# Kernel tuning notes

Measured on AMD Instinct MI355X. Metric: run time of the kernel, lower is better.

The kernel has to match this reference:

```python
import jax, jax.numpy as jnp
import numpy as np

DIM = 512
HEADS = 8
HEAD_DIM = 64
MAX_FREQ = 256.0


def axial_freqs(H, W, head_dim, max_freq=MAX_FREQ):
    # rotary-embedding-torch: per-axis rotary dim = head_dim // 2, freqs_for='pixel'
    r = head_dim // 2
    base = jnp.linspace(1.0, max_freq / 2.0, r // 2) * jnp.pi  # (r/2,)
    ph = jnp.linspace(-1.0, 1.0, H)
    pw = jnp.linspace(-1.0, 1.0, W)
    fh = jnp.repeat(ph[:, None] * base[None, :], 2, axis=-1)  # (H, r) interleaved repeat
    fw = jnp.repeat(pw[:, None] * base[None, :], 2, axis=-1)  # (W, r)
    fh = jnp.broadcast_to(fh[:, None, :], (H, W, r))
    fw = jnp.broadcast_to(fw[None, :, :], (H, W, r))
    return jnp.concatenate([fh, fw], axis=-1)  # (H, W, head_dim)


def rotate_half(t):
    # interleaved pairs: (x1, x2) -> (-x2, x1)
    shp = t.shape
    t = t.reshape(*shp[:-1], -1, 2)
    return jnp.stack((-t[..., 1], t[..., 0]), axis=-1).reshape(shp)


def apply_rope(t, freqs):
    # freqs: (H, W, d) broadcast over (BT, h, H, W, d)
    return t * jnp.cos(freqs) + rotate_half(t) * jnp.sin(freqs)


def setup_inputs() -> dict:
    key = jax.random.key(0)
    k1, k2, k3 = jax.random.split(key, 3)
    B, T, H, W, D = 2, 8, 32, 32, DIM
    inner = HEADS * HEAD_DIM
    x = jax.random.normal(k1, (B, T, H, W, D), dtype=jnp.float32)
    w_qkv = jax.random.normal(k2, (3 * inner, D), dtype=jnp.float32) * (D ** -0.5)
    w_out = jax.random.normal(k3, (D, inner), dtype=jnp.float32) * (inner ** -0.5)
    b_out = jnp.zeros((D,), dtype=jnp.float32)
    return {"x": x, "w_qkv": w_qkv, "w_out": w_out, "b_out": b_out}


def reference(x, w_qkv, w_out, b_out):
    B, T, H, W, D = x.shape
    h, d = HEADS, HEAD_DIM
    qkv = jnp.einsum('bthwc,fc->bthwf', x, w_qkv)  # (B,T,H,W,3*inner)
    q, k, v = jnp.split(qkv, 3, axis=-1)

    def to_heads(t):
        # B T H W (h d) -> (B T) h H W d
        t = t.reshape(B * T, H, W, h, d)
        return jnp.transpose(t, (0, 3, 1, 2, 4))

    q, k, v = to_heads(q), to_heads(k), to_heads(v)
    freqs = axial_freqs(H, W, d)
    q = apply_rope(q, freqs)
    k = apply_rope(k, freqs)

    q = q.reshape(B * T, h, H * W, d)
    k = k.reshape(B * T, h, H * W, d)
    v = v.reshape(B * T, h, H * W, d)

    scale = d ** -0.5
    logits = jnp.einsum('bhnd,bhmd->bhnm', q, k) * scale
    attn = jax.nn.softmax(logits, axis=-1)
    out = jnp.einsum('bhnm,bhmd->bhnd', attn, v)  # (BT, h, HW, d)

    # (B T) h (H W) d -> B T H W (h d)
    out = out.reshape(B, T, h, H, W, d)
    out = jnp.transpose(out, (0, 1, 3, 4, 2, 5)).reshape(B, T, H, W, h * d)
    return jnp.einsum('bthwf,df->bthwd', out, w_out) + b_out
```

## Files before the change

### kernel.cpp

```cpp
#include <hip/hip_runtime.h>
#include <math.h>

#define NH 8
#define HD 64
#define NSEQ 1024
#define DMODEL 512
#define F3 1536
#define NTOK 16384
#define BH 128
#define KVP 72
#define TP 136
#define QSCALE 0.1803368867f

typedef __attribute__((ext_vector_type(8))) short bf16x8;
typedef __attribute__((ext_vector_type(4))) float f32x4;
typedef __attribute__((ext_vector_type(16))) float f32x16;
typedef __attribute__((ext_vector_type(4))) unsigned int u32x4;
#define MFMA16(a, b, c) __builtin_amdgcn_mfma_f32_16x16x32_bf16(a, b, c, 0, 0, 0)
#define MFMA32(a, b, c) __builtin_amdgcn_mfma_f32_32x32x16_bf16(a, b, c, 0, 0, 0)

__device__ __forceinline__ float freq_of(int j) {
    return 3.14159265358979323846f * (1.0f + (float)j * (127.0f / 15.0f));
}
__device__ __forceinline__ unsigned short bf16_hi(float x) {
    unsigned u = __builtin_bit_cast(unsigned, x);
    return (unsigned short)(u >> 16);
}
__device__ __forceinline__ unsigned short bf16_rtn(float x) {
    unsigned u = __builtin_bit_cast(unsigned, x);
    return (unsigned short)((u + 0x7FFF + ((u >> 16) & 1)) >> 16);
}
__device__ __forceinline__ float bf16_tofloat(unsigned short h) {
    unsigned u = ((unsigned)h) << 16;
    return __builtin_bit_cast(float, u);
}
__device__ __forceinline__ int swz(int r) { return (r & 3) ^ ((r >> 2) & 3); }

__global__ __launch_bounds__(256) void split_kernel(
        const float* __restrict__ src, unsigned short* __restrict__ hi,
        unsigned short* __restrict__ lo) {
    const int i = blockIdx.x * 256 + threadIdx.x;
    const float4 v = ((const float4*)src)[i];
    ushort4 h, l;
    h.x = bf16_hi(v.x); l.x = bf16_hi(v.x - bf16_tofloat(h.x));
    h.y = bf16_hi(v.y); l.y = bf16_hi(v.y - bf16_tofloat(h.y));
    h.z = bf16_hi(v.z); l.z = bf16_hi(v.z - bf16_tofloat(h.z));
    h.w = bf16_hi(v.w); l.w = bf16_hi(v.w - bf16_tofloat(h.w));
    ((ushort4*)hi)[i] = h;
    ((ushort4*)lo)[i] = l;
}
__global__ __launch_bounds__(256) void cvt_kernel(
        const float* __restrict__ src, unsigned short* __restrict__ dst) {
    const int i = blockIdx.x * 256 + threadIdx.x;
    const float4 v = ((const float4*)src)[i];
    ((ushort4*)dst)[i] = make_ushort4(bf16_rtn(v.x), bf16_rtn(v.y),
                                      bf16_rtn(v.z), bf16_rtn(v.w));
}

template<int PLANES, int NREP>
__device__ __forceinline__ void gemm_reg_pipe(
        const unsigned short* __restrict__ a_hi, const unsigned short* __restrict__ a_lo,
        const unsigned short* __restrict__ b_bf,
        char* lds, int m0, int f0, int t, f32x4 (&acc)[NREP][4][4]) {
    const int w = t >> 6, lane = t & 63, l15 = lane & 15, quad = lane >> 4;
    const int mw = (w & 1) * 64, nw = (w >> 1) * 64;
    const int APL = PLANES - 1;
    const int NPL = APL + NREP;
    const int STAGE = NPL * 4096;
    const int r = t >> 1;
    const int g0 = (t & 1) * 2;

    uint4 regs[NPL][2];
    auto load_regs = [&](int kt) {
        const int k0 = kt * 32;
        #pragma unroll
        for (int p = 0; p < NPL; p++) {
            const unsigned short* src = (p < APL) ? (p == 0 ? a_hi : a_lo) : b_bf;
            const int row0 = (p < APL) ? m0 : (f0 + (p - APL) * 128);
            const unsigned short* g = src + (size_t)(row0 + r) * DMODEL + k0 + g0 * 8;
            regs[p][0] = *(const uint4*)g;
            regs[p][1] = *(const uint4*)(g + 8);
        }
    };
    auto store_lds = [&](int stage) {
        unsigned short* S = (unsigned short*)lds + stage * STAGE;
        const int s0 = ((g0 ^ swz(r))) * 8;
        const int s1 = (((g0 + 1) ^ swz(r))) * 8;
        #pragma unroll
        for (int p = 0; p < NPL; p++) {
            unsigned short* Sp = S + p * 4096 + r * 32;
            *(uint4*)&Sp[s0] = regs[p][0];
            *(uint4*)&Sp[s1] = regs[p][1];
        }
    };

    load_regs(0);
    store_lds(0);
    for (int kt = 0; kt < 16; kt++) {
        __syncthreads();
        if (kt < 15) load_regs(kt + 1);
        const unsigned short* S = (const unsigned short*)lds + (kt & 1) * STAGE;
        bf16x8 ah[4], al[4];
        #pragma unroll
        for (int mt = 0; mt < 4; mt++) {
            const int rr = mw + mt * 16 + l15;
            const int off = rr * 32 + (quad ^ swz(rr)) * 8;
            ah[mt] = *(const bf16x8*)&S[off];
            if (APL == 2) al[mt] = *(const bf16x8*)&S[4096 + off];
        }
        #pragma unroll
        for (int nr = 0; nr < NREP; nr++) {
            bf16x8 bb[4];
            #pragma unroll
            for (int nt = 0; nt < 4; nt++) {
                const int rr = nw + nt * 16 + l15;
                bb[nt] = *(const bf16x8*)&S[(APL + nr) * 4096 + rr * 32
                                            + (quad ^ swz(rr)) * 8];
            }
            #pragma unroll
            for (int mt = 0; mt < 4; mt++)
                #pragma unroll
                for (int nt = 0; nt < 4; nt++) {
                    acc[nr][mt][nt] = MFMA16(ah[mt], bb[nt], acc[nr][mt][nt]);
                    if (APL == 2) acc[nr][mt][nt] = MFMA16(al[mt], bb[nt], acc[nr][mt][nt]);
                }
        }
        if (kt < 15) store_lds((kt + 1) & 1);
    }
    __syncthreads();
}

__global__ __launch_bounds__(256, 2) void qkv_mfma_kernel(
        const unsigned short* __restrict__ x_hi, const unsigned short* __restrict__ x_lo,
        const unsigned short* __restrict__ wq_bf,
        unsigned short* __restrict__ q_bf, unsigned short* __restrict__ k_bf,
        unsigned short* __restrict__ v_th) {
    __shared__ __align__(16) char lds[65536 + 4608];
    unsigned short* T = (unsigned short*)lds;
    float* t_cy = (float*)(lds + 65536);
    float* t_sy = t_cy + 64;
    float* t_cx = t_sy + 64;
    float* t_sx = t_cx + 512;

    const int m0 = blockIdx.x * 128;
    const int f0 = blockIdx.y * 256;
    const int t = threadIdx.x;
    const int w = t >> 6, lane = t & 63, l15 = lane & 15, quad = lane >> 4;
    const int mw = (w & 1) * 64, nw = (w >> 1) * 64;
    const int sel = f0 >> 9;
    const int bt = m0 >> 10;
    const int n0 = m0 & 1023;

    if (sel != 2) {
        for (int idx = t; idx < 576; idx += 256) {
            if (idx < 64) {
                const int yi = idx >> 4, j = idx & 15;
                const float pos = -1.0f + (float)((n0 >> 5) + yi) * (2.0f / 31.0f);
                float sv, cv; sincosf(pos * freq_of(j), &sv, &cv);
                t_sy[idx] = sv; t_cy[idx] = cv;
            } else {
                const int k2 = idx - 64, xi = k2 >> 4, j = k2 & 15;
                const float pos = -1.0f + (float)xi * (2.0f / 31.0f);
                float sv, cv; sincosf(pos * freq_of(j), &sv, &cv);
                t_sx[k2] = sv; t_cx[k2] = cv;
            }
        }
    }
    __syncthreads();

    f32x4 acc[2][4][4];
    #pragma unroll
    for (int nr = 0; nr < 2; nr++)
        #pragma unroll
        for (int mt = 0; mt < 4; mt++)
            #pragma unroll
            for (int nt = 0; nt < 4; nt++) acc[nr][mt][nt] = (f32x4){0.f, 0.f, 0.f, 0.f};

    gemm_reg_pipe<3, 2>(x_hi, x_lo, wq_bf, lds, m0, f0, t, acc);

    #pragma unroll
    for (int nr = 0; nr < 2; nr++) {
        const int fs = f0 + nr * 128;
        if (sel != 2) {
            const float post = (sel == 0) ? QSCALE : 1.0f;
            #pragma unroll
            for (int mt = 0; mt < 4; mt++)
                #pragma unroll
                for (int nt = 0; nt < 4; nt++)
                    #pragma unroll
                    for (int rr = 0; rr < 4; rr++) {
                        const int ml = mw + mt * 16 + quad * 4 + rr;
                        const int dd = (nw + nt * 16 + l15) & 63;
                        const int j0 = (dd & 31) >> 1;
                        float c, s;
                        if (dd < 32) { c = t_cy[(ml >> 5) * 16 + j0]; s = t_sy[(ml >> 5) * 16 + j0]; }
                        else         { c = t_cx[(ml & 31) * 16 + j0]; s = t_sx[(ml & 31) * 16 + j0]; }
                        const float v = acc[nr][mt][nt][rr];
                        const float pv = __shfl_xor(v, 1);
                        acc[nr][mt][nt][rr] =
                            ((l15 & 1) ? (v * c + pv * s) : (v * c - pv * s)) * post;
                    }
        }

        if (sel == 2) {
            #pragma unroll
            for (int mt = 0; mt < 4; mt++)
                #pragma unroll
                for (int nt = 0; nt < 4; nt++) {
                    const int fl = nw + nt * 16 + l15;
                    const int mlb = mw + mt * 16 + quad * 4;
                    ushort4 pk = make_ushort4(
                        bf16_rtn(acc[nr][mt][nt][0]), bf16_rtn(acc[nr][mt][nt][1]),
                        bf16_rtn(acc[nr][mt][nt][2]), bf16_rtn(acc[nr][mt][nt][3]));
                    *(ushort4*)&T[fl * TP + mlb] = pk;
                }
        } else {
            #pragma unroll
            for (int mt = 0; mt < 4; mt++)
                #pragma unroll
                for (int nt = 0; nt < 4; nt++)
                    #pragma unroll
                    for (int rr = 0; rr < 4; rr++) {
                        const int ml = mw + mt * 16 + quad * 4 + rr;
                        const int fl = nw + nt * 16 + l15;
                        T[ml * TP + fl] = bf16_rtn(acc[nr][mt][nt][rr]);
                    }
        }
        __syncthreads();
        if (sel == 2) {
            #pragma unroll
            for (int p = 0; p < 8; p++) {
                const int idx = p * 256 + t;
                const int fl = idx >> 4, g8 = (idx & 15) * 8;
                const int head = ((fs + fl) >> 6) & 7;
                *(uint4*)(v_th + ((size_t)(bt * NH + head) * HD + ((fs + fl) & 63)) * NSEQ
                          + n0 + g8) = *(const uint4*)&T[fl * TP + g8];
            }
        } else {
            unsigned short* dst = (sel == 0) ? q_bf : k_bf;
            #pragma unroll
            for (int p = 0; p < 8; p++) {
                const int idx = p * 256 + t;
                const int ml = idx >> 4, g8 = (idx & 15) * 8;
                const int head = ((fs + g8) >> 6) & 7;
                *(uint4*)(dst + ((size_t)(bt * NH + head) * NSEQ + n0 + ml) * HD
                          + ((fs + g8) & 63)) = *(const uint4*)&T[ml * TP + g8];
            }
        }
        __syncthreads();
    }
}

__global__ __launch_bounds__(256, 3) void attn_kernel(
        const unsigned short* __restrict__ q_bf, const unsigned short* __restrict__ k_bf,
        const unsigned short* __restrict__ v_th,
        unsigned short* __restrict__ o_bf) {
    __shared__ unsigned short Ks[2][64 * KVP];
    __shared__ unsigned short Vs[2][64 * KVP];

    const int bh = blockIdx.x;
    const int qt = blockIdx.y;
    const int t = threadIdx.x;
    const int w = t >> 6;
    const int lane = t & 63;
    const int l31 = lane & 31;
    const int hi = lane >> 5;

    const size_t bh_nd = (size_t)bh * NSEQ * HD;
    const size_t bh_dn = (size_t)bh * HD * NSEQ;

    bf16x8 qfB[4];
    {
        const size_t rbase = bh_nd + (size_t)(qt * 128 + w * 32 + l31) * HD + hi * 8;
        #pragma unroll
        for (int ds = 0; ds < 4; ds++)
            qfB[ds] = *(const bf16x8*)(q_bf + rbase + ds * 16);
    }

    uint4 kr[2], vr[2];
    auto load_kv = [&](int kt) {
        #pragma unroll
        for (int p = 0; p < 2; p++) {
            const int cc = t + p * 256;
            const int r = cc >> 3, off8 = (cc & 7) * 8;
            kr[p] = *(const uint4*)(k_bf + bh_nd + (size_t)(kt * 64 + r) * HD + off8);
            vr[p] = *(const uint4*)(v_th + bh_dn + (size_t)r * NSEQ + kt * 64 + off8);
        }
    };
    auto store_kv = [&](int st) {
        #pragma unroll
        for (int p = 0; p < 2; p++) {
            const int cc = t + p * 256;
            const int r = cc >> 3, off8 = (cc & 7) * 8;
            *(uint4*)&Ks[st][r * KVP + off8] = kr[p];
            *(uint4*)&Vs[st][r * KVP + off8] = vr[p];
        }
    };

    const bf16x8 ones = {(short)0x3F80, (short)0x3F80, (short)0x3F80, (short)0x3F80,
                         (short)0x3F80, (short)0x3F80, (short)0x3F80, (short)0x3F80};

    f32x16 o_acc[2], l_acc;
    #pragma unroll
    for (int i = 0; i < 16; i++) {
        o_acc[0][i] = 0.f; o_acc[1][i] = 0.f; l_acc[i] = 0.f;
    }

    load_kv(0);
    store_kv(0);
    for (int kt = 0; kt < 16; kt++) {
        __syncthreads();
        if (kt < 15) load_kv(kt + 1);
        const unsigned short* K = Ks[kt & 1];
        const unsigned short* V = Vs[kt & 1];

        #pragma unroll
        for (int nt2 = 0; nt2 < 2; nt2++) {
            f32x16 s;
            #pragma unroll
            for (int i = 0; i < 16; i++) s[i] = 0.f;
            #pragma unroll
            for (int ds = 0; ds < 4; ds++) {
                const bf16x8 kb =
                    *(const bf16x8*)&K[(nt2 * 32 + l31) * KVP + ds * 16 + hi * 8];
                s = MFMA32(kb, qfB[ds], s);
            }

            unsigned wv[8];
            #pragma unroll
            for (int i = 0; i < 8; i++) {
                const float p0 = exp2f(s[2 * i]);
                const float p1 = exp2f(s[2 * i + 1]);
                asm("v_cvt_pk_bf16_f32 %0, %1, %2" : "=v"(wv[i]) : "v"(p0), "v"(p1));
            }
            asm volatile("v_permlane32_swap_b32 %0, %1" : "+v"(wv[0]), "+v"(wv[2]));
            asm volatile("v_permlane32_swap_b32 %0, %1" : "+v"(wv[1]), "+v"(wv[3]));
            asm volatile("v_permlane32_swap_b32 %0, %1" : "+v"(wv[4]), "+v"(wv[6]));
            asm volatile("v_permlane32_swap_b32 %0, %1" : "+v"(wv[5]), "+v"(wv[7]));

            #pragma unroll
            for (int k2 = 0; k2 < 2; k2++) {
                const u32x4 paw = {wv[k2 * 4 + 0], wv[k2 * 4 + 1],
                                   wv[k2 * 4 + 2], wv[k2 * 4 + 3]};
                const bf16x8 pa = __builtin_bit_cast(bf16x8, paw);
                const int kstep = nt2 * 2 + k2;
                l_acc = MFMA32(pa, ones, l_acc);
                #pragma unroll
                for (int dt = 0; dt < 2; dt++) {
                    const bf16x8 vb =
                        *(const bf16x8*)&V[(dt * 32 + l31) * KVP + kstep * 16 + hi * 8];
                    o_acc[dt] = MFMA32(pa, vb, o_acc[dt]);
                }
            }
        }
        if (kt < 15) store_kv((kt + 1) & 1);
    }

    __syncthreads();
    unsigned short* Osh = &Ks[0][0];
    #pragma unroll
    for (int r = 0; r < 16; r++) {
        const float inv = 1.0f / l_acc[r];
        const int row = w * 32 + (r & 3) + 8 * (r >> 2) + 4 * hi;
        #pragma unroll
        for (int dt = 0; dt < 2; dt++)
            Osh[row * KVP + dt * 32 + l31] = bf16_rtn(o_acc[dt][r] * inv);
    }
    __syncthreads();
    const int btq = bh >> 3, head = bh & 7;
    #pragma unroll
    for (int p = 0; p < 4; p++) {
        const int idx = p * 256 + t;
        const int row = idx >> 3, g8 = (idx & 7) * 8;
        *(uint4*)(o_bf + ((size_t)(btq * NSEQ + qt * 128 + row)) * DMODEL
                  + head * HD + g8) = *(const uint4*)&Osh[row * KVP + g8];
    }
}

__global__ __launch_bounds__(256, 3) void proj_mfma_kernel(
        const unsigned short* __restrict__ o_bf,
        const unsigned short* __restrict__ wo_bf,
        const float* __restrict__ b_out, float* __restrict__ out) {
    __shared__ __align__(16) char lds[32768];

    const int m0 = blockIdx.x * 128;
    const int f0 = blockIdx.y * 128;
    const int t = threadIdx.x;
    const int w = t >> 6, lane = t & 63, l15 = lane & 15, quad = lane >> 4;
    const int mw = (w & 1) * 64, nw = (w >> 1) * 64;

    f32x4 acc[1][4][4];
    #pragma unroll
    for (int mt = 0; mt < 4; mt++)
        #pragma unroll
        for (int nt = 0; nt < 4; nt++) acc[0][mt][nt] = (f32x4){0.f, 0.f, 0.f, 0.f};

    gemm_reg_pipe<2, 1>(o_bf, o_bf, wo_bf, lds, m0, f0, t, acc);

    float bias_v[4];
    #pragma unroll
    for (int nt = 0; nt < 4; nt++) bias_v[nt] = b_out[f0 + nw + nt * 16 + l15];
    #pragma unroll
    for (int mt = 0; mt < 4; mt++)
        #pragma unroll
        for (int nt = 0; nt < 4; nt++)
            #pragma unroll
            for (int rr = 0; rr < 4; rr++) {
                const int m = m0 + mw + mt * 16 + quad * 4 + rr;
                out[(size_t)m * DMODEL + f0 + nw + nt * 16 + l15] =
                    acc[0][mt][nt][rr] + bias_v[nt];
            }
}

extern "C" void kernel_launch(void* const* d_in, const int* in_sizes, int n_in,
                              void* d_out, int out_size, void* d_ws, size_t ws_size,
                              hipStream_t stream) {
    const float* x  = (const float*)d_in[0];
    const float* wq = (const float*)d_in[1];
    const float* wo = (const float*)d_in[2];
    const float* bo = (const float*)d_in[3];
    float* out = (float*)d_out;

    const size_t per = (size_t)BH * NSEQ * HD;
    unsigned short* x_hi = (unsigned short*)d_ws;
    unsigned short* x_lo = x_hi + per;
    unsigned short* q_bf = x_lo + per;
    unsigned short* k_bf = q_bf + per;
    unsigned short* v_th = k_bf + per;
    unsigned short* wq_bf = v_th + per;
    unsigned short* wo_bf = wq_bf + (size_t)F3 * DMODEL;
    unsigned short* o_bf = x_hi;

    split_kernel<<<dim3((int)(per / 1024)), 256, 0, stream>>>(x, x_hi, x_lo);
    cvt_kernel<<<dim3(F3 * DMODEL / 1024), 256, 0, stream>>>(wq, wq_bf);
    cvt_kernel<<<dim3(DMODEL * DMODEL / 1024), 256, 0, stream>>>(wo, wo_bf);
    qkv_mfma_kernel<<<dim3(NTOK / 128, F3 / 256), 256, 0, stream>>>(
        x_hi, x_lo, wq_bf, q_bf, k_bf, v_th);
    attn_kernel<<<dim3(BH, 8), 256, 0, stream>>>(
        q_bf, k_bf, v_th, o_bf);
    proj_mfma_kernel<<<dim3(NTOK / 128, DMODEL / 128), 256, 0, stream>>>(
        o_bf, wo_bf, bo, out);
}
```

Baseline: 252.9 us.

## Load K/V fragments directly from global memory instead of LDS staging in attention

The attention kernel no longer stages K and V tiles through double-buffered shared memory with block-wide barriers. Each wave now loads its MFMA operands straight from global memory (relying on L2/L1 caching) and wraps the MFMA sections in s_setprio. With LDS use reduced to the output staging buffer, the occupancy hint goes from 3 to 4 blocks per CU. The trade-off is that every wave re-reads the same K/V data from cache, and global-load latency is exposed without explicit prefetch.

```diff
diff --git a/kernel.cpp b/kernel.cpp
--- a/kernel.cpp
+++ b/kernel.cpp
@@ -251,12 +251,11 @@
     }
 }
 
-__global__ __launch_bounds__(256, 3) void attn_kernel(
+__global__ __launch_bounds__(256, 4) void attn_kernel(
         const unsigned short* __restrict__ q_bf, const unsigned short* __restrict__ k_bf,
         const unsigned short* __restrict__ v_th,
         unsigned short* __restrict__ o_bf) {
-    __shared__ unsigned short Ks[2][64 * KVP];
-    __shared__ unsigned short Vs[2][64 * KVP];
+    __shared__ unsigned short Osh[128 * KVP];
 
     const int bh = blockIdx.x;
     const int qt = blockIdx.y;
@@ -277,25 +276,8 @@
             qfB[ds] = *(const bf16x8*)(q_bf + rbase + ds * 16);
     }
 
-    uint4 kr[2], vr[2];
-    auto load_kv = [&](int kt) {
-        #pragma unroll
-        for (int p = 0; p < 2; p++) {
-            const int cc = t + p * 256;
-            const int r = cc >> 3, off8 = (cc & 7) * 8;
-            kr[p] = *(const uint4*)(k_bf + bh_nd + (size_t)(kt * 64 + r) * HD + off8);
-            vr[p] = *(const uint4*)(v_th + bh_dn + (size_t)r * NSEQ + kt * 64 + off8);
-        }
-    };
-    auto store_kv = [&](int st) {
-        #pragma unroll
-        for (int p = 0; p < 2; p++) {
-            const int cc = t + p * 256;
-            const int r = cc >> 3, off8 = (cc & 7) * 8;
-            *(uint4*)&Ks[st][r * KVP + off8] = kr[p];
-            *(uint4*)&Vs[st][r * KVP + off8] = vr[p];
-        }
-    };
+    const unsigned short* Kl = k_bf + bh_nd + (size_t)l31 * HD + hi * 8;
+    const unsigned short* Vl = v_th + bh_dn + (size_t)l31 * NSEQ + hi * 8;
 
     const bf16x8 ones = {(short)0x3F80, (short)0x3F80, (short)0x3F80, (short)0x3F80,
                          (short)0x3F80, (short)0x3F80, (short)0x3F80, (short)0x3F80};
@@ -306,25 +288,31 @@
         o_acc[0][i] = 0.f; o_acc[1][i] = 0.f; l_acc[i] = 0.f;
     }
 
-    load_kv(0);
-    store_kv(0);
+    #pragma unroll 2
     for (int kt = 0; kt < 16; kt++) {
-        __syncthreads();
-        if (kt < 15) load_kv(kt + 1);
-        const unsigned short* K = Ks[kt & 1];
-        const unsigned short* V = Vs[kt & 1];
-
+        const int n0k = kt * 64;
         #pragma unroll
         for (int nt2 = 0; nt2 < 2; nt2++) {
+            bf16x8 kb[4];
+            #pragma unroll
+            for (int ds = 0; ds < 4; ds++)
+                kb[ds] = *(const bf16x8*)(Kl + (size_t)(n0k + nt2 * 32) * HD + ds * 16);
+
+            __builtin_amdgcn_s_setprio(1);
             f32x16 s;
             #pragma unroll
             for (int i = 0; i < 16; i++) s[i] = 0.f;
             #pragma unroll
-            for (int ds = 0; ds < 4; ds++) {
-                const bf16x8 kb =
-                    *(const bf16x8*)&K[(nt2 * 32 + l31) * KVP + ds * 16 + hi * 8];
-                s = MFMA32(kb, qfB[ds], s);
-            }
+            for (int ds = 0; ds < 4; ds++) s = MFMA32(kb[ds], qfB[ds], s);
+            __builtin_amdgcn_s_setprio(0);
+
+            bf16x8 vb[2][2];
+            #pragma unroll
+            for (int k2 = 0; k2 < 2; k2++)
+                #pragma unroll
+                for (int dt = 0; dt < 2; dt++)
+                    vb[k2][dt] = *(const bf16x8*)(Vl + (size_t)(dt * 32) * NSEQ
+                                  + n0k + (nt2 * 2 + k2) * 16);
 
             unsigned wv[8];
             #pragma unroll
@@ -338,26 +326,21 @@
             asm volatile("v_permlane32_swap_b32 %0, %1" : "+v"(wv[4]), "+v"(wv[6]));
             asm volatile("v_permlane32_swap_b32 %0, %1" : "+v"(wv[5]), "+v"(wv[7]));
 
+            __builtin_amdgcn_s_setprio(1);
             #pragma unroll
             for (int k2 = 0; k2 < 2; k2++) {
                 const u32x4 paw = {wv[k2 * 4 + 0], wv[k2 * 4 + 1],
                                    wv[k2 * 4 + 2], wv[k2 * 4 + 3]};
                 const bf16x8 pa = __builtin_bit_cast(bf16x8, paw);
-                const int kstep = nt2 * 2 + k2;
                 l_acc = MFMA32(pa, ones, l_acc);
                 #pragma unroll
-                for (int dt = 0; dt < 2; dt++) {
-                    const bf16x8 vb =
-                        *(const bf16x8*)&V[(dt * 32 + l31) * KVP + kstep * 16 + hi * 8];
-                    o_acc[dt] = MFMA32(pa, vb, o_acc[dt]);
-                }
-            }
-        }
-        if (kt < 15) store_kv((kt + 1) & 1);
-    }
-
-    __syncthreads();
-    unsigned short* Osh = &Ks[0][0];
+                for (int dt = 0; dt < 2; dt++)
+                    o_acc[dt] = MFMA32(pa, vb[k2][dt], o_acc[dt]);
+            }
+            __builtin_amdgcn_s_setprio(0);
+        }
+    }
+
     #pragma unroll
     for (int r = 0; r < 16; r++) {
         const float inv = 1.0f / l_acc[r];
```

New measurement: 283.3 us. 1.12x slower.
